# Kernel tuning notes

Hardware: AMD Instinct MI355X
Metric: run time of the kernel (lower is better)

The kernel has to match this reference:

```python
import jax, jax.numpy as jnp
import numpy as np

BS, N_CTX, N_HEADS, WIDTH = 2, 2048, 8, 32
N_TOK = 512


def setup_inputs() -> dict:
    key = jax.random.key(0)
    kq, kk, kv, ki = jax.random.split(key, 4)
    q = jax.random.normal(kq, (BS, N_CTX, N_HEADS, WIDTH), dtype=jnp.float32)
    k = jax.random.normal(kk, (BS, N_CTX, N_HEADS, WIDTH), dtype=jnp.float32)
    v = jax.random.normal(kv, (BS, N_CTX, N_HEADS, WIDTH), dtype=jnp.float32)
    indx = jnp.sort(jax.random.randint(ki, (N_TOK,), 0, N_CTX, dtype=jnp.int64))
    return {"q": q, "k": k, "v": v, "indx": indx}


def reference(q, k, v, indx):
    # q, k, v: (bs, n_ctx, n_heads, width); indx: (n_tok,) token ids to attend over
    n_tok = indx.shape[0]
    scale = jnp.float32(1.0 / np.sqrt(n_tok))
    qg = q[:, indx]  # (bs, n_tok, h, w) -- gathered tokens (t axis in torch code)
    kg = k[:, indx]  # (bs, n_tok, h, w) -- gathered tokens (s axis in torch code)
    vg = v[:, indx]  # (bs, n_tok, h, w)
    # L1 distance scores: ww[b,s,t,h] = scale * sum_w |q[b,indx[t],h,w] - k[b,indx[s],h,w]|
    diff = jnp.abs(qg[:, None, :, :, :] - kg[:, :, None, :, :])  # (bs, s, t, h, w)
    scores = -scale * jnp.sum(diff, axis=-1)  # (bs, s, t, h)
    attn = jax.nn.softmax(scores, axis=2)  # softmax over t (matches torch softmax(-1) on (b,h,s,t))
    # out[b,s,h,w] = sum_t attn[b,s,t,h] * v[b,indx[t],h,w]
    out = jnp.einsum('bsth,bthw->bshw', attn, vg)
    return out
```

## Files before the change

kernel.cpp:

```cpp
#include <hip/hip_runtime.h>

#define NCTX 2048
#define NH   8
#define WD   32
#define NTOK 512

static constexpr float SCALE = 0.04419417382415922f;

template<int S>
__global__ __launch_bounds__(512, 6) void l1attn_main(
    const float* __restrict__ q, const float* __restrict__ k,
    const float* __restrict__ v, const int* __restrict__ indx,
    float* __restrict__ dst ) {
  constexpr int JSPAN = NTOK / S;
  constexpr int NWIN  = JSPAN / 128;
  __shared__ int   indxS[NTOK];
  __shared__ float ldsQ[128 * 32];
  __shared__ float ldsV[128 * 32];
  __shared__ float accS[32 * 33];
  __shared__ float lS[32];

  const int tid = threadIdx.x;
  const int bid = blockIdx.x;
  const int pr  = bid / S;
  const int jw  = bid % S;
  const int plane = pr >> 4;
  const int rg    = pr & 15;
  const int b     = plane >> 3;
  const int h     = plane & 7;

  indxS[tid] = indx[tid];
  for (int i = tid; i < 32 * 33; i += 512) accS[i] = 0.f;
  if (tid < 32) lS[tid] = 0.f;
  __syncthreads();

  const float* qb = q + ((size_t)b * NCTX * NH) * WD + h * WD;
  const float* vb = v + ((size_t)b * NCTX * NH) * WD + h * WD;
  const float* kb = k + ((size_t)b * NCTX * NH) * WD + h * WD;

  const int lane  = tid & 63;
  const int wave  = __builtin_amdgcn_readfirstlane(tid >> 6);
  const int r     = lane & 31;
  const int whalf = lane >> 5;

  float kg[16];
  {
    const int s = rg * 32 + r;
    const float4* kr =
        (const float4*)(kb + (size_t)indxS[s] * (NH * WD) + whalf * 16);
#pragma unroll
    for (int i = 0; i < 4; ++i) {
      float4 t = kr[i];
      kg[4*i+0] = t.x; kg[4*i+1] = t.y; kg[4*i+2] = t.z; kg[4*i+3] = t.w;
    }
  }

  float acc[16];
#pragma unroll
  for (int i = 0; i < 16; ++i) acc[i] = 0.f;
  float l = 0.f;

  for (int wnd = 0; wnd < NWIN; ++wnd) {
    if (wnd) __syncthreads();

    const int tok0 = jw * JSPAN + wnd * 128;
    for (int i = tid; i < 128 * 8; i += 512) {
      const int t = i >> 3, sg = i & 7;
      const int tok = indxS[tok0 + t];
      ((float4*)ldsQ)[i] = ((const float4*)(qb + (size_t)tok * (NH * WD)))[sg];
      ((float4*)ldsV)[i] = ((const float4*)(vb + (size_t)tok * (NH * WD)))[sg];
    }
    __syncthreads();

    const int j0 = wave * 16;
    for (int jj = 0; jj < 16; ++jj) {
      const float* qrow = ldsQ + (j0 + jj) * 32 + whalf * 16;
      const float* vrow = ldsV + (j0 + jj) * 32 + whalf * 16;

      float d0, d1, d2, d3;
      {
        float4 t = ((const float4*)qrow)[0];
        d0 = fabsf(t.x - kg[0]); d1 = fabsf(t.y - kg[1]);
        d2 = fabsf(t.z - kg[2]); d3 = fabsf(t.w - kg[3]);
      }
#pragma unroll
      for (int i = 1; i < 4; ++i) {
        float4 t = ((const float4*)qrow)[i];
        d0 += fabsf(t.x - kg[4*i+0]);
        d1 += fabsf(t.y - kg[4*i+1]);
        d2 += fabsf(t.z - kg[4*i+2]);
        d3 += fabsf(t.w - kg[4*i+3]);
      }
      float d = (d0 + d1) + (d2 + d3);
      d += __shfl_xor(d, 32, 64);
      const float p = __expf(-SCALE * d);
      l += p;
#pragma unroll
      for (int i = 0; i < 4; ++i) {
        float4 t = ((const float4*)vrow)[i];
        acc[4*i+0] = fmaf(p, t.x, acc[4*i+0]);
        acc[4*i+1] = fmaf(p, t.y, acc[4*i+1]);
        acc[4*i+2] = fmaf(p, t.z, acc[4*i+2]);
        acc[4*i+3] = fmaf(p, t.w, acc[4*i+3]);
      }
    }
  }

#pragma unroll
  for (int w = 0; w < 16; ++w)
    atomicAdd(&accS[r * 33 + whalf * 16 + w], acc[w]);
  if (whalf == 0) atomicAdd(&lS[r], l);
  __syncthreads();

  if (S > 1) {
    float* wsB = dst + (size_t)bid * 1056;
    for (int i = tid; i < 1024; i += 512)
      wsB[i] = accS[(i >> 5) * 33 + (i & 31)];
    if (tid < 32) wsB[1024 + tid] = lS[tid];
  } else {
    for (int i = tid; i < 1024; i += 512) {
      const int rr = i >> 5, w = i & 31;
      dst[(((size_t)b * NTOK + rg * 32 + rr) * NH + h) * WD + w] =
          accS[rr * 33 + w] / lS[rr];
    }
  }
}

template<int S>
__global__ __launch_bounds__(1024) void l1attn_combine(
    const float* __restrict__ ws, float* __restrict__ out) {
  const int gid = blockIdx.x * 1024 + threadIdx.x;
  const int w  = gid & 31;
  const int r  = (gid >> 5) & 31;
  const int pr = gid >> 10;
  const float* base = ws + (size_t)pr * S * 1056;
  float a = 0.f, ls = 0.f;
#pragma unroll
  for (int jwi = 0; jwi < S; ++jwi) {
    a  += base[jwi * 1056 + r * 32 + w];
    ls += base[jwi * 1056 + 1024 + r];
  }
  const int plane = pr >> 4, rg = pr & 15;
  const int b = plane >> 3, h = plane & 7;
  out[(((size_t)b * NTOK + rg * 32 + r) * NH + h) * WD + w] = a / ls;
}

extern "C" void kernel_launch(void* const* d_in, const int* in_sizes, int n_in,
                              void* d_out, int out_size, void* d_ws, size_t ws_size,
                              hipStream_t stream) {
  const float* q    = (const float*)d_in[0];
  const float* k    = (const float*)d_in[1];
  const float* v    = (const float*)d_in[2];
  const int*   indx = (const int*)d_in[3];
  float*       out  = (float*)d_out;

  const size_t need4 = (size_t)1024 * 1056 * sizeof(float);
  const size_t need2 = (size_t)512  * 1056 * sizeof(float);
  if (ws_size >= need4) {
    hipLaunchKernelGGL((l1attn_main<4>), dim3(1024), dim3(512), 0, stream,
                       q, k, v, indx, (float*)d_ws);
    hipLaunchKernelGGL((l1attn_combine<4>), dim3(256), dim3(1024), 0, stream,
                       (const float*)d_ws, out);
  } else if (ws_size >= need2) {
    hipLaunchKernelGGL((l1attn_main<2>), dim3(512), dim3(512), 0, stream,
                       q, k, v, indx, (float*)d_ws);
    hipLaunchKernelGGL((l1attn_combine<2>), dim3(256), dim3(1024), 0, stream,
                       (const float*)d_ws, out);
  } else {
    hipLaunchKernelGGL((l1attn_main<1>), dim3(256), dim3(512), 0, stream,
                       q, k, v, indx, out);
  }
}
```

Measured before the change: 64.96 us.

## Replace LDS staging with double-buffered direct global loads via inline asm

Drops the shared-memory staging of gathered Q/V rows and the per-window barriers. Each wave now streams its own token range straight from global memory into registers, using hand-issued dwordx4 loads with two register buffers and explicit vmcnt waits so loads for the next token overlap compute on the current one. Occupancy hint is lowered from 6 to 4 to make room for the extra registers. The risk is more redundant global/L2 traffic, since each wave loads rows previously shared via LDS, and fragile inline-asm scheduling.

```diff
diff --git a/kernel.cpp b/kernel.cpp
--- a/kernel.cpp
+++ b/kernel.cpp
@@ -7,16 +7,59 @@
 
 static constexpr float SCALE = 0.04419417382415922f;
 
+#define ISSUE8(qp, vp, a0,a1,a2,a3,a4,a5,a6,a7)            \
+  asm volatile(                                            \
+    "global_load_dwordx4 %0, %8, off\n\t"                  \
+    "global_load_dwordx4 %1, %8, off offset:16\n\t"        \
+    "global_load_dwordx4 %2, %8, off offset:32\n\t"        \
+    "global_load_dwordx4 %3, %8, off offset:48\n\t"        \
+    "global_load_dwordx4 %4, %9, off\n\t"                  \
+    "global_load_dwordx4 %5, %9, off offset:16\n\t"        \
+    "global_load_dwordx4 %6, %9, off offset:32\n\t"        \
+    "global_load_dwordx4 %7, %9, off offset:48\n\t"        \
+    : "=&v"(a0),"=&v"(a1),"=&v"(a2),"=&v"(a3),             \
+      "=&v"(a4),"=&v"(a5),"=&v"(a6),"=&v"(a7)              \
+    : "v"(qp), "v"(vp))
+
+#define WAITV(N)                                           \
+  do {                                                     \
+    asm volatile("s_waitcnt vmcnt(" #N ")" ::: "memory");  \
+    __builtin_amdgcn_sched_barrier(0);                     \
+  } while (0)
+
+#define BODY(q0,q1,q2,q3, v0,v1,v2,v3)                                      \
+  do {                                                                      \
+    float d0, d1, d2, d3;                                                   \
+    d0  = fabsf(q0.x - kg[ 0]); d1  = fabsf(q0.y - kg[ 1]);                 \
+    d2  = fabsf(q0.z - kg[ 2]); d3  = fabsf(q0.w - kg[ 3]);                 \
+    d0 += fabsf(q1.x - kg[ 4]); d1 += fabsf(q1.y - kg[ 5]);                 \
+    d2 += fabsf(q1.z - kg[ 6]); d3 += fabsf(q1.w - kg[ 7]);                 \
+    d0 += fabsf(q2.x - kg[ 8]); d1 += fabsf(q2.y - kg[ 9]);                 \
+    d2 += fabsf(q2.z - kg[10]); d3 += fabsf(q2.w - kg[11]);                 \
+    d0 += fabsf(q3.x - kg[12]); d1 += fabsf(q3.y - kg[13]);                 \
+    d2 += fabsf(q3.z - kg[14]); d3 += fabsf(q3.w - kg[15]);                 \
+    float d = (d0 + d1) + (d2 + d3);                                        \
+    d += __shfl_xor(d, 32, 64);              \
+    const float p = __expf(-SCALE * d);        \
+    l += p;                                                                 \
+    acc[ 0] = fmaf(p, v0.x, acc[ 0]); acc[ 1] = fmaf(p, v0.y, acc[ 1]);     \
+    acc[ 2] = fmaf(p, v0.z, acc[ 2]); acc[ 3] = fmaf(p, v0.w, acc[ 3]);     \
+    acc[ 4] = fmaf(p, v1.x, acc[ 4]); acc[ 5] = fmaf(p, v1.y, acc[ 5]);     \
+    acc[ 6] = fmaf(p, v1.z, acc[ 6]); acc[ 7] = fmaf(p, v1.w, acc[ 7]);     \
+    acc[ 8] = fmaf(p, v2.x, acc[ 8]); acc[ 9] = fmaf(p, v2.y, acc[ 9]);     \
+    acc[10] = fmaf(p, v2.z, acc[10]); acc[11] = fmaf(p, v2.w, acc[11]);     \
+    acc[12] = fmaf(p, v3.x, acc[12]); acc[13] = fmaf(p, v3.y, acc[13]);     \
+    acc[14] = fmaf(p, v3.z, acc[14]); acc[15] = fmaf(p, v3.w, acc[15]);     \
+  } while (0)
+
 template<int S>
-__global__ __launch_bounds__(512, 6) void l1attn_main(
+__global__ __launch_bounds__(512, 4) void l1attn_main(
     const float* __restrict__ q, const float* __restrict__ k,
     const float* __restrict__ v, const int* __restrict__ indx,
     float* __restrict__ dst ) {
   constexpr int JSPAN = NTOK / S;
-  constexpr int NWIN  = JSPAN / 128;
+  constexpr int JPW   = JSPAN / 8;
   __shared__ int   indxS[NTOK];
-  __shared__ float ldsQ[128 * 32];
-  __shared__ float ldsV[128 * 32];
   __shared__ float accS[32 * 33];
   __shared__ float lS[32];
 
@@ -34,20 +77,19 @@
   if (tid < 32) lS[tid] = 0.f;
   __syncthreads();
 
-  const float* qb = q + ((size_t)b * NCTX * NH) * WD + h * WD;
-  const float* vb = v + ((size_t)b * NCTX * NH) * WD + h * WD;
-  const float* kb = k + ((size_t)b * NCTX * NH) * WD + h * WD;
-
   const int lane  = tid & 63;
   const int wave  = __builtin_amdgcn_readfirstlane(tid >> 6);
   const int r     = lane & 31;
   const int whalf = lane >> 5;
 
+  const float* qb = q + ((size_t)b * NCTX * NH + h) * WD + whalf * 16;
+  const float* vb = v + ((size_t)b * NCTX * NH + h) * WD + whalf * 16;
+  const float* kb = k + ((size_t)b * NCTX * NH + h) * WD + whalf * 16;
+
   float kg[16];
   {
     const int s = rg * 32 + r;
-    const float4* kr =
-        (const float4*)(kb + (size_t)indxS[s] * (NH * WD) + whalf * 16);
+    const float4* kr = (const float4*)(kb + (size_t)indxS[s] * (NH * WD));
 #pragma unroll
     for (int i = 0; i < 4; ++i) {
       float4 t = kr[i];
@@ -60,50 +102,41 @@
   for (int i = 0; i < 16; ++i) acc[i] = 0.f;
   float l = 0.f;
 
-  for (int wnd = 0; wnd < NWIN; ++wnd) {
-    if (wnd) __syncthreads();
-
-    const int tok0 = jw * JSPAN + wnd * 128;
-    for (int i = tid; i < 128 * 8; i += 512) {
-      const int t = i >> 3, sg = i & 7;
-      const int tok = indxS[tok0 + t];
-      ((float4*)ldsQ)[i] = ((const float4*)(qb + (size_t)tok * (NH * WD)))[sg];
-      ((float4*)ldsV)[i] = ((const float4*)(vb + (size_t)tok * (NH * WD)))[sg];
-    }
-    __syncthreads();
-
-    const int j0 = wave * 16;
-    for (int jj = 0; jj < 16; ++jj) {
-      const float* qrow = ldsQ + (j0 + jj) * 32 + whalf * 16;
-      const float* vrow = ldsV + (j0 + jj) * 32 + whalf * 16;
-
-      float d0, d1, d2, d3;
-      {
-        float4 t = ((const float4*)qrow)[0];
-        d0 = fabsf(t.x - kg[0]); d1 = fabsf(t.y - kg[1]);
-        d2 = fabsf(t.z - kg[2]); d3 = fabsf(t.w - kg[3]);
-      }
-#pragma unroll
-      for (int i = 1; i < 4; ++i) {
-        float4 t = ((const float4*)qrow)[i];
-        d0 += fabsf(t.x - kg[4*i+0]);
-        d1 += fabsf(t.y - kg[4*i+1]);
-        d2 += fabsf(t.z - kg[4*i+2]);
-        d3 += fabsf(t.w - kg[4*i+3]);
-      }
-      float d = (d0 + d1) + (d2 + d3);
-      d += __shfl_xor(d, 32, 64);
-      const float p = __expf(-SCALE * d);
-      l += p;
-#pragma unroll
-      for (int i = 0; i < 4; ++i) {
-        float4 t = ((const float4*)vrow)[i];
-        acc[4*i+0] = fmaf(p, t.x, acc[4*i+0]);
-        acc[4*i+1] = fmaf(p, t.y, acc[4*i+1]);
-        acc[4*i+2] = fmaf(p, t.z, acc[4*i+2]);
-        acc[4*i+3] = fmaf(p, t.w, acc[4*i+3]);
-      }
-    }
+  const int jb = jw * JSPAN + wave * JPW;
+
+  float4 Aq0, Aq1, Aq2, Aq3, Av0, Av1, Av2, Av3;
+  float4 Bq0, Bq1, Bq2, Bq3, Bv0, Bv1, Bv2, Bv3;
+
+  {
+    const int tok0 = indxS[jb];
+    ISSUE8(qb + (size_t)tok0 * 256, vb + (size_t)tok0 * 256,
+           Aq0, Aq1, Aq2, Aq3, Av0, Av1, Av2, Av3);
+  }
+
+  for (int jj = 0; jj < JPW - 2; jj += 2) {
+    {
+      const int t1 = indxS[jb + jj + 1];
+      ISSUE8(qb + (size_t)t1 * 256, vb + (size_t)t1 * 256,
+             Bq0, Bq1, Bq2, Bq3, Bv0, Bv1, Bv2, Bv3);
+      WAITV(8);
+      BODY(Aq0, Aq1, Aq2, Aq3, Av0, Av1, Av2, Av3);
+    }
+    {
+      const int t2 = indxS[jb + jj + 2];
+      ISSUE8(qb + (size_t)t2 * 256, vb + (size_t)t2 * 256,
+             Aq0, Aq1, Aq2, Aq3, Av0, Av1, Av2, Av3);
+      WAITV(8);
+      BODY(Bq0, Bq1, Bq2, Bq3, Bv0, Bv1, Bv2, Bv3);
+    }
+  }
+  {
+    const int t1 = indxS[jb + JPW - 1];
+    ISSUE8(qb + (size_t)t1 * 256, vb + (size_t)t1 * 256,
+           Bq0, Bq1, Bq2, Bq3, Bv0, Bv1, Bv2, Bv3);
+    WAITV(8);
+    BODY(Aq0, Aq1, Aq2, Aq3, Av0, Av1, Av2, Av3);
+    WAITV(0);
+    BODY(Bq0, Bq1, Bq2, Bq3, Bv0, Bv1, Bv2, Bv3);
   }
 
 #pragma unroll
```

New measurement: 137.9 us. 112% more time.
